# Kernel tuning notes

Hardware: AMD Instinct MI355X
Metric: run time of the kernel (lower is better)

The kernel has to match this reference:

```python
import jax, jax.numpy as jnp
import numpy as np

L, B, D = 2048, 8, 768
EPS_BN = 1e-5
EPS_LN = 1e-5
SCALE = 1.0 / float(np.sqrt(D))


def setup_inputs() -> dict:
    key = jax.random.key(0)
    ks = jax.random.split(key, 8)
    f32 = jnp.float32
    return {
        "x_a": jax.random.normal(ks[0], (L, B, D), dtype=f32),
        "x_v": jax.random.normal(ks[1], (L, B, D), dtype=f32),
        "x": jax.random.normal(ks[2], (L, B, D), dtype=f32),
        # conv1x1 (audio branch): weight [out_ch, in_ch], bias [out_ch]
        "W_a": jax.random.normal(ks[3], (D, D), dtype=f32) * 0.02,
        "b_a": jnp.zeros((D,), f32),
        "bn_a_g": jnp.ones((D,), f32),
        "bn_a_b": jnp.zeros((D,), f32),
        "prelu_a": jnp.full((1,), 0.25, f32),
        # conv1x1 (video branch)
        "W_v": jax.random.normal(ks[4], (D, D), dtype=f32) * 0.02,
        "b_v": jnp.zeros((D,), f32),
        "bn_v_g": jnp.ones((D,), f32),
        "bn_v_b": jnp.zeros((D,), f32),
        "prelu_v": jnp.full((1,), 0.25, f32),
        # final LayerNorm affine
        "ln_g": jnp.ones((D,), f32),
        "ln_b": jnp.zeros((D,), f32),
    }


def _branch(q, kv, W, b, bn_g, bn_b, alpha):
    # q: [B, L, D] queries; kv: [B, Lm, D] keys == values (cross-modal)
    attn = jax.nn.softmax(jnp.einsum('bld,bmd->blm', q, kv) * SCALE, axis=-1)
    ctx = jnp.einsum('blm,bmd->bld', attn, kv)            # [B, L, D]
    # Conv1d(kernel=1) over channel dim D == per-position linear
    y = jnp.einsum('bld,ed->ble', ctx, W) + b             # [B, L, D]
    # BatchNorm1d in training mode: batch stats over (B, L) per channel, biased var
    mean = jnp.mean(y, axis=(0, 1))
    var = jnp.var(y, axis=(0, 1))
    y = (y - mean) * jax.lax.rsqrt(var + EPS_BN) * bn_g + bn_b
    # PReLU (single shared alpha)
    return jnp.where(y > 0, y, alpha * y)


def reference(x_a, x_v, x, W_a, b_a, bn_a_g, bn_a_b, prelu_a,
              W_v, b_v, bn_v_g, bn_v_b, prelu_v, ln_g, ln_b):
    xa = jnp.swapaxes(x_a, 0, 1)   # [B, La, D]
    xv = jnp.swapaxes(x_v, 0, 1)   # [B, Lv, D]
    xq = jnp.swapaxes(x, 0, 1)     # [B, L, D]

    res_a = _branch(xq, xa, W_a, b_a, bn_a_g, bn_a_b, prelu_a)
    res_v = _branch(xq, xv, W_v, b_v, bn_v_g, bn_v_b, prelu_v)

    out = xq + res_a + res_v
    out = jnp.swapaxes(out, 0, 1)  # back to [L, B, D]

    mu = jnp.mean(out, axis=-1, keepdims=True)
    var = jnp.var(out, axis=-1, keepdims=True)
    return (out - mu) * jax.lax.rsqrt(var + EPS_LN) * ln_g + ln_b
```

## Files before the change

kernel.cpp:

```cpp
#include <hip/hip_runtime.h>
#include <stdint.h>

#define LL 2048
#define BB 8
#define DD 768
#define NROWS (LL*BB)
#define QKSCALE 0.03608439182435161f
#define EP 72

typedef __attribute__((ext_vector_type(8))) short short8;
typedef __attribute__((ext_vector_type(4))) float f32x4;
typedef unsigned short u16;
typedef unsigned int u32;

__device__ __forceinline__ float bf2f(u16 u) {
    union { u32 u; float f; } c; c.u = ((u32)u) << 16; return c.f;
}
__device__ __forceinline__ u16 f2bf(float f) {
    union { float f; u32 u; } c; c.f = f;
    return (u16)((c.u + 0x8000u) >> 16);
}

__global__ __launch_bounds__(256)
void cvt_kernel(const float* __restrict__ s0, u16* __restrict__ d0,
                const float* __restrict__ s1, u16* __restrict__ d1,
                const float* __restrict__ s2, u16* __restrict__ d2,
                const float* __restrict__ s3, u16* __restrict__ d3,
                const float* __restrict__ s4, u16* __restrict__ d4,
                int nbig4, int nsmall4)
{
    const float* src; u16* dst; int n4;
    switch (blockIdx.y) {
        case 0: src = s0; dst = d0; n4 = nbig4; break;
        case 1: src = s1; dst = d1; n4 = nbig4; break;
        case 2: src = s2; dst = d2; n4 = nbig4; break;
        case 3: src = s3; dst = d3; n4 = nsmall4; break;
        default: src = s4; dst = d4; n4 = nsmall4; break;
    }
    for (int i = blockIdx.x * 256 + threadIdx.x; i < n4; i += gridDim.x * 256) {
        float4 v = *(const float4*)&src[i * 4];
        ushort4 o;
        o.x = f2bf(v.x); o.y = f2bf(v.y); o.z = f2bf(v.z); o.w = f2bf(v.w);
        *(ushort4*)&dst[i * 4] = o;
    }
}

__device__ __forceinline__ void gll16(const u16* g, u16* l) {
    __builtin_amdgcn_global_load_lds((const __attribute__((address_space(1))) u32*)g,
                                     (__attribute__((address_space(3))) u32*)l, 16, 0, 0);
}

template<int EPI>
__global__ __launch_bounds__(512, 2)
void gemm_bt256(const u16* __restrict__ A, int lda, long astr,
                const u16* __restrict__ B, int ldb, long bstr,
                u16* __restrict__ C, long cstr, int ldc,
                int K, int sw,
                float* __restrict__ lsum,
                const float* __restrict__ bias,
                float* __restrict__ stats)
{
    __shared__ u16 lds[65536];

    const int tid = threadIdx.x;
    const int z = blockIdx.z;
    const int flat = blockIdx.y * gridDim.x + blockIdx.x;
    const int per = sw * gridDim.x;
    const int bm = (flat / per) * sw + (flat % sw);
    const int bn = (flat % per) / sw;
    const int m0 = bm * 256, n0 = bn * 256;

    const u16* Ab = A + (size_t)z * astr + (size_t)m0 * lda;
    const u16* Bb = B + (size_t)z * bstr + (size_t)n0 * ldb;
    u16* Cb = C + (size_t)z * cstr;

    const int lane = tid & 63, w = tid >> 6;
    const int wm = w >> 2, wn = w & 3;
    const int lr = lane & 15, lg = lane >> 4;

    const int ar0 = tid >> 2;
    const int ar1 = ar0 + 128;
    const int ag0 = (tid & 3) ^ ((ar0 >> 1) & 3);
    const int ag1 = (tid & 3) ^ ((ar1 >> 1) & 3);
    const u16* gA0 = Ab + (size_t)ar0 * lda + ag0 * 8;
    const u16* gA1 = Ab + (size_t)ar1 * lda + ag1 * 8;
    const u16* gB0 = Bb + (size_t)ar0 * ldb + ag0 * 8;
    const u16* gB1 = Bb + (size_t)ar1 * ldb + ag1 * 8;
    const int lA0 = tid * 8;
    const int lA1 = tid * 8 + 4096;
    const int lB0 = 8192 + tid * 8;
    const int lB1 = 12288 + tid * 8;

    const int swz = (lr >> 1) & 3;
    const int aoff = (wm * 128 + lr) * 32 + ((lg ^ swz) * 8);
    const int boff = 8192 + (wn * 64 + lr) * 32 + ((lg ^ swz) * 8);

    f32x4 acc[8][4];
    const f32x4 zz = {0.f, 0.f, 0.f, 0.f};
    #pragma unroll
    for (int i = 0; i < 8; ++i)
        #pragma unroll
        for (int j = 0; j < 4; ++j) acc[i][j] = zz;

    const int nt = K >> 5;

    {
        u16* b0 = lds;
        u16* b1 = lds + 16384;
        gll16(gA0, b0 + lA0); gll16(gA1, b0 + lA1);
        gll16(gB0, b0 + lB0); gll16(gB1, b0 + lB1);
        gll16(gA0 + 32, b1 + lA0); gll16(gA1 + 32, b1 + lA1);
        gll16(gB0 + 32, b1 + lB0); gll16(gB1 + 32, b1 + lB1);
    }
    asm volatile("s_waitcnt vmcnt(4)" ::: "memory");
    asm volatile("s_barrier" ::: "memory");

    for (int t = 0; t < nt; ++t) {
        const int cb = (t & 3) * 16384;
        const int sb = ((t + 2) & 3) * 16384;
        const int kt2 = (t + 2) * 32;
        const bool pre = (t + 2 < nt);
        short8 af[4], bf[4];

        #pragma unroll
        for (int mi = 0; mi < 4; ++mi) af[mi] = *(const short8*)&lds[cb + aoff + mi * 512];
        #pragma unroll
        for (int ni = 0; ni < 4; ++ni) bf[ni] = *(const short8*)&lds[cb + boff + ni * 512];
        if (pre) { gll16(gA0 + kt2, lds + sb + lA0); gll16(gA1 + kt2, lds + sb + lA1); }
        asm volatile("s_barrier" ::: "memory");
        __builtin_amdgcn_s_setprio(1);
        #pragma unroll
        for (int mi = 0; mi < 4; ++mi)
            #pragma unroll
            for (int ni = 0; ni < 4; ++ni)
                acc[mi][ni] = __builtin_amdgcn_mfma_f32_16x16x32_bf16(af[mi], bf[ni], acc[mi][ni], 0, 0, 0);
        __builtin_amdgcn_s_setprio(0);

        #pragma unroll
        for (int mi = 0; mi < 4; ++mi) af[mi] = *(const short8*)&lds[cb + aoff + 2048 + mi * 512];
        if (pre) { gll16(gB0 + kt2, lds + sb + lB0); gll16(gB1 + kt2, lds + sb + lB1); }
        if (t < nt - 2) asm volatile("s_waitcnt vmcnt(4)" ::: "memory");
        else            asm volatile("s_waitcnt vmcnt(0)" ::: "memory");
        asm volatile("s_barrier" ::: "memory");
        __builtin_amdgcn_s_setprio(1);
        #pragma unroll
        for (int mi = 0; mi < 4; ++mi)
            #pragma unroll
            for (int ni = 0; ni < 4; ++ni)
                acc[mi + 4][ni] = __builtin_amdgcn_mfma_f32_16x16x32_bf16(af[mi], bf[ni], acc[mi + 4][ni], 0, 0, 0);
        __builtin_amdgcn_s_setprio(0);
    }

    asm volatile("s_barrier" ::: "memory");
    u16* eb = lds + w * 4608;

    float invl[8][4]; float bcol[4];
    if constexpr (EPI == 2) {
        #pragma unroll
        for (int mi = 0; mi < 8; ++mi)
            #pragma unroll
            for (int r = 0; r < 4; ++r)
                invl[mi][r] = 1.0f / lsum[z * 2048 + m0 + wm * 128 + mi * 16 + lg * 4 + r];
        #pragma unroll
        for (int ni = 0; ni < 4; ++ni)
            bcol[ni] = bias[n0 + wn * 64 + ni * 16 + lr];
    }
    float csum[4] = {0, 0, 0, 0}, csq[4] = {0, 0, 0, 0};

    #pragma unroll
    for (int half = 0; half < 2; ++half) {
        #pragma unroll
        for (int mi = 0; mi < 4; ++mi) {
            const int MI = half * 4 + mi;
            float rsum[4] = {0, 0, 0, 0};
            #pragma unroll
            for (int ni = 0; ni < 4; ++ni) {
                #pragma unroll
                for (int r = 0; r < 4; ++r) {
                    float v = acc[MI][ni][r];
                    if constexpr (EPI == 1) { v = __expf(v * QKSCALE); rsum[r] += v; }
                    if constexpr (EPI == 2) { v = v * invl[MI][r] + bcol[ni]; csum[ni] += v; csq[ni] += v * v; }
                    eb[(mi * 16 + lg * 4 + r) * EP + ni * 16 + lr] = f2bf(v);
                }
            }
            if constexpr (EPI == 1) {
                #pragma unroll
                for (int r = 0; r < 4; ++r) {
                    float s = rsum[r];
                    s += __shfl_xor(s, 1); s += __shfl_xor(s, 2);
                    s += __shfl_xor(s, 4); s += __shfl_xor(s, 8);
                    if (lr == 0)
                        atomicAdd(&lsum[z * 2048 + m0 + wm * 128 + MI * 16 + lg * 4 + r], s);
                }
            }
        }
        #pragma unroll
        for (int c = 0; c < 8; ++c) {
            int row = c * 8 + (lane >> 3);
            short8 v = *(const short8*)&eb[row * EP + (lane & 7) * 8];
            *(short8*)&Cb[(size_t)(m0 + wm * 128 + half * 64 + row) * ldc + n0 + wn * 64 + (lane & 7) * 8] = v;
        }
    }
    if constexpr (EPI == 2) {
        #pragma unroll
        for (int ni = 0; ni < 4; ++ni) {
            float s = csum[ni], q = csq[ni];
            s += __shfl_xor(s, 16); s += __shfl_xor(s, 32);
            q += __shfl_xor(q, 16); q += __shfl_xor(q, 32);
            if (lg == 0) {
                atomicAdd(&stats[n0 + wn * 64 + ni * 16 + lr], s);
                atomicAdd(&stats[DD + n0 + wn * 64 + ni * 16 + lr], q);
            }
        }
    }
}

__global__ void bn_params(const float* __restrict__ stats_a, const float* __restrict__ stats_v,
                          const float* __restrict__ g_a, const float* __restrict__ be_a,
                          const float* __restrict__ g_v, const float* __restrict__ be_v,
                          float* __restrict__ bnp_a, float* __restrict__ bnp_v)
{
    const int e = threadIdx.x;
    const float* st = (blockIdx.x == 0) ? stats_a : stats_v;
    const float* g  = (blockIdx.x == 0) ? g_a  : g_v;
    const float* be = (blockIdx.x == 0) ? be_a : be_v;
    float* bnp = (blockIdx.x == 0) ? bnp_a : bnp_v;
    float mean = st[e] * (1.0f / NROWS);
    float var  = st[DD + e] * (1.0f / NROWS) - mean * mean;
    float scale = g[e] * rsqrtf(var + 1e-5f);
    bnp[e]      = scale;
    bnp[DD + e] = be[e] - mean * scale;
}

__global__ __launch_bounds__(256)
void final_kernel(const float* __restrict__ x,
                  const u16* __restrict__ y_a, const u16* __restrict__ y_v,
                  const float* __restrict__ bnp_a, const float* __restrict__ bnp_v,
                  const float* __restrict__ pra, const float* __restrict__ prv,
                  const float* __restrict__ lng, const float* __restrict__ lnb,
                  float* __restrict__ out)
{
    const int n = blockIdx.x;
    const int tid = threadIdx.x;
    __shared__ float vrow[DD];
    __shared__ float reds[4], reds2[4];
    const float aa = pra[0];
    const float av = prv[0];
    const size_t base = (size_t)n * DD;
    float s = 0.f, s2 = 0.f;
    for (int e = tid; e < DD; e += 256) {
        float ya = bf2f(y_a[base + e]) * bnp_a[e] + bnp_a[DD + e];
        ya = ya > 0.f ? ya : aa * ya;
        float yv = bf2f(y_v[base + e]) * bnp_v[e] + bnp_v[DD + e];
        yv = yv > 0.f ? yv : av * yv;
        float v = x[base + e] + ya + yv;
        vrow[e] = v;
        s += v; s2 += v * v;
    }
    for (int off = 32; off > 0; off >>= 1) { s += __shfl_xor(s, off); s2 += __shfl_xor(s2, off); }
    const int wv = tid >> 6;
    if ((tid & 63) == 0) { reds[wv] = s; reds2[wv] = s2; }
    __syncthreads();
    float ts  = reds[0] + reds[1] + reds[2] + reds[3];
    float ts2 = reds2[0] + reds2[1] + reds2[2] + reds2[3];
    float mean = ts * (1.0f / DD);
    float var  = ts2 * (1.0f / DD) - mean * mean;
    float rstd = rsqrtf(var + 1e-5f);
    for (int e = tid; e < DD; e += 256) {
        float o = (vrow[e] - mean) * rstd * lng[e] + lnb[e];
        out[base + e] = o;
    }
}

extern "C" void kernel_launch(void* const* d_in, const int* in_sizes, int n_in,
                              void* d_out, int out_size, void* d_ws, size_t ws_size,
                              hipStream_t stream)
{
    const float* x_a    = (const float*)d_in[0];
    const float* x_v    = (const float*)d_in[1];
    const float* x      = (const float*)d_in[2];
    const float* W_a    = (const float*)d_in[3];
    const float* b_a    = (const float*)d_in[4];
    const float* bn_a_g = (const float*)d_in[5];
    const float* bn_a_b = (const float*)d_in[6];
    const float* pr_a   = (const float*)d_in[7];
    const float* W_v    = (const float*)d_in[8];
    const float* b_v    = (const float*)d_in[9];
    const float* bn_v_g = (const float*)d_in[10];
    const float* bn_v_b = (const float*)d_in[11];
    const float* pr_v   = (const float*)d_in[12];
    const float* ln_g   = (const float*)d_in[13];
    const float* ln_b   = (const float*)d_in[14];

    float* stats_a = (float*)d_ws;
    float* stats_v = stats_a + 1536;
    float* bnp_a   = stats_v + 1536;
    float* bnp_v   = bnp_a + 1536;
    float* lsum    = bnp_v + 1536;
    u16* xq_bf = (u16*)(lsum + 16 * 2048);
    u16* xa_bf = xq_bf + (size_t)NROWS * DD;
    u16* xv_bf = xa_bf + (size_t)NROWS * DD;
    u16* Wa_bf = xv_bf + (size_t)NROWS * DD;
    u16* Wv_bf = Wa_bf + (size_t)DD * DD;
    u16* UT    = Wv_bf + (size_t)DD * DD;
    u16* y_a = xa_bf;
    u16* y_v = xv_bf;
    size_t fixed_bytes = (size_t)((char*)UT - (char*)d_ws);

    int nb = 1;
    for (int cand = 8; cand >= 1; cand >>= 1) {
        size_t need = fixed_bytes + (size_t)cand * (3145728ull + 8388608ull);
        if (need <= ws_size) { nb = cand; break; }
    }
    u16* P = UT + (size_t)nb * (768 * 2048);

    hipMemsetAsync(stats_a, 0, (4 * 1536 + 16 * 2048) * sizeof(float), stream);

    cvt_kernel<<<dim3(3072, 5), 256, 0, stream>>>(
        x, xq_bf, x_a, xa_bf, x_v, xv_bf, W_a, Wa_bf, W_v, Wv_bf,
        NROWS * DD / 4, DD * DD / 4);

    const u16*   KVs[2]   = { xa_bf, xv_bf };
    const u16*   Ws[2]    = { Wa_bf, Wv_bf };
    const float* BIs[2]   = { b_a, b_v };
    u16*         Ys[2]    = { y_a, y_v };
    float*       STs[2]   = { stats_a, stats_v };

    for (int br = 0; br < 2; ++br) {
        const u16* kv = KVs[br];
        for (int c0 = 0; c0 < 8; c0 += nb) {
            float* lsum_bc = (nb == 8) ? (lsum + br * 8 * 2048) : lsum;
            if (nb != 8)
                hipMemsetAsync(lsum, 0, (size_t)nb * 2048 * sizeof(float), stream);
            gemm_bt256<0><<<dim3(8, 3, nb), 512, 0, stream>>>(
                Ws[br], DD, 0, kv + c0 * DD, BB * DD, DD,
                UT, (long)768 * 2048, 2048, DD, 3, nullptr, nullptr, nullptr);
            gemm_bt256<1><<<dim3(8, 8, nb), 512, 0, stream>>>(
                xq_bf + c0 * DD, BB * DD, DD, kv + c0 * DD, BB * DD, DD,
                P, (long)2048 * 2048, 2048, DD, 4, lsum_bc, nullptr, nullptr);
            gemm_bt256<2><<<dim3(3, 8, nb), 512, 0, stream>>>(
                P, 2048, (long)2048 * 2048, UT, 2048, (long)768 * 2048,
                Ys[br] + (size_t)c0 * DD, DD, BB * DD, 2048, 4, lsum_bc, BIs[br], STs[br]);
        }
    }

    bn_params<<<2, 768, 0, stream>>>(stats_a, stats_v, bn_a_g, bn_a_b, bn_v_g, bn_v_b, bnp_a, bnp_v);
    final_kernel<<<NROWS, 256, 0, stream>>>(x, y_a, y_v, bnp_a, bnp_v, pr_a, pr_v, ln_g, ln_b,
                                            (float*)d_out);
}
```

Measured before the change: 539.3 us.

## Software-pipeline LDS fragment loads across k-steps and drop one barrier

```diff
diff --git a/kernel.cpp b/kernel.cpp
--- a/kernel.cpp
+++ b/kernel.cpp
@@ -104,6 +104,8 @@
 
     const int nt = K >> 5;
 
+    short8 a1[4], a2[4], bE[4], bO[4];
+
     {
         u16* b0 = lds;
         u16* b1 = lds + 16384;
@@ -114,42 +116,60 @@
     }
     asm volatile("s_waitcnt vmcnt(4)" ::: "memory");
     asm volatile("s_barrier" ::: "memory");
-
-    for (int t = 0; t < nt; ++t) {
-        const int cb = (t & 3) * 16384;
-        const int sb = ((t + 2) & 3) * 16384;
-        const int kt2 = (t + 2) * 32;
-        const bool pre = (t + 2 < nt);
-        short8 af[4], bf[4];
-
-        #pragma unroll
-        for (int mi = 0; mi < 4; ++mi) af[mi] = *(const short8*)&lds[cb + aoff + mi * 512];
-        #pragma unroll
-        for (int ni = 0; ni < 4; ++ni) bf[ni] = *(const short8*)&lds[cb + boff + ni * 512];
-        if (pre) { gll16(gA0 + kt2, lds + sb + lA0); gll16(gA1 + kt2, lds + sb + lA1); }
-        asm volatile("s_barrier" ::: "memory");
-        __builtin_amdgcn_s_setprio(1);
-        #pragma unroll
-        for (int mi = 0; mi < 4; ++mi)
-            #pragma unroll
-            for (int ni = 0; ni < 4; ++ni)
-                acc[mi][ni] = __builtin_amdgcn_mfma_f32_16x16x32_bf16(af[mi], bf[ni], acc[mi][ni], 0, 0, 0);
-        __builtin_amdgcn_s_setprio(0);
-
-        #pragma unroll
-        for (int mi = 0; mi < 4; ++mi) af[mi] = *(const short8*)&lds[cb + aoff + 2048 + mi * 512];
-        if (pre) { gll16(gB0 + kt2, lds + sb + lB0); gll16(gB1 + kt2, lds + sb + lB1); }
-        if (t < nt - 2) asm volatile("s_waitcnt vmcnt(4)" ::: "memory");
-        else            asm volatile("s_waitcnt vmcnt(0)" ::: "memory");
-        asm volatile("s_barrier" ::: "memory");
-        __builtin_amdgcn_s_setprio(1);
-        #pragma unroll
-        for (int mi = 0; mi < 4; ++mi)
-            #pragma unroll
-            for (int ni = 0; ni < 4; ++ni)
-                acc[mi + 4][ni] = __builtin_amdgcn_mfma_f32_16x16x32_bf16(af[mi], bf[ni], acc[mi + 4][ni], 0, 0, 0);
-        __builtin_amdgcn_s_setprio(0);
-    }
+    #pragma unroll
+    for (int mi = 0; mi < 4; ++mi) a1[mi] = *(const short8*)&lds[aoff + mi * 512];
+    #pragma unroll
+    for (int ni = 0; ni < 4; ++ni) bE[ni] = *(const short8*)&lds[boff + ni * 512];
+
+#define TILE_STEP(T, BC, BN)                                                            \
+    {                                                                                   \
+        const int cb_ = ((T) & 3) * 16384;                                              \
+        const int sb_ = (((T) + 2) & 3) * 16384;                                        \
+        const int kt2_ = ((T) + 2) * 32;                                                \
+        _Pragma("unroll")                                                               \
+        for (int mi = 0; mi < 4; ++mi)                                                  \
+            a2[mi] = *(const short8*)&lds[cb_ + aoff + 2048 + mi * 512];                \
+        if ((T) + 2 < nt) {                                                             \
+            gll16(gA0 + kt2_, lds + sb_ + lA0);                                         \
+            gll16(gA1 + kt2_, lds + sb_ + lA1);                                         \
+        }                                                                               \
+        __builtin_amdgcn_s_setprio(1);                                                  \
+        _Pragma("unroll")                                                               \
+        for (int mi = 0; mi < 4; ++mi)                                                  \
+            _Pragma("unroll")                                                           \
+            for (int ni = 0; ni < 4; ++ni)                                              \
+                acc[mi][ni] = __builtin_amdgcn_mfma_f32_16x16x32_bf16(a1[mi], BC[ni], acc[mi][ni], 0, 0, 0); \
+        __builtin_amdgcn_s_setprio(0);                                                  \
+        if ((T) + 2 < nt) {                                                             \
+            gll16(gB0 + kt2_, lds + sb_ + lB0);                                         \
+            gll16(gB1 + kt2_, lds + sb_ + lB1);                                         \
+        }                                                                               \
+        if ((T) < nt - 2) { asm volatile("s_waitcnt vmcnt(4)" ::: "memory"); }          \
+        else              { asm volatile("s_waitcnt vmcnt(0)" ::: "memory"); }          \
+        asm volatile("s_barrier" ::: "memory");                                         \
+        if ((T) + 1 < nt) {                                                             \
+            const int nb_ = (((T) + 1) & 3) * 16384;                                    \
+            _Pragma("unroll")                                                           \
+            for (int mi = 0; mi < 4; ++mi)                                              \
+                a1[mi] = *(const short8*)&lds[nb_ + aoff + mi * 512];                   \
+            _Pragma("unroll")                                                           \
+            for (int ni = 0; ni < 4; ++ni)                                              \
+                BN[ni] = *(const short8*)&lds[nb_ + boff + ni * 512];                   \
+        }                                                                               \
+        __builtin_amdgcn_s_setprio(1);                                                  \
+        _Pragma("unroll")                                                               \
+        for (int mi = 0; mi < 4; ++mi)                                                  \
+            _Pragma("unroll")                                                           \
+            for (int ni = 0; ni < 4; ++ni)                                              \
+                acc[mi + 4][ni] = __builtin_amdgcn_mfma_f32_16x16x32_bf16(a2[mi], BC[ni], acc[mi + 4][ni], 0, 0, 0); \
+        __builtin_amdgcn_s_setprio(0);                                                  \
+    }
+
+    for (int t = 0; t < nt; t += 2) {
+        TILE_STEP(t, bE, bO)
+        TILE_STEP(t + 1, bO, bE)
+    }
+#undef TILE_STEP
 
     asm volatile("s_barrier" ::: "memory");
     u16* eb = lds + w * 4608;
```

Measured after the change: 571.0 us. 5.9% more time.

## Shrink GEMM tile to 256x128 with 4 waves and double-buffered LDS

Applied to the files above, without the earlier changes.

```diff
diff --git a/kernel.cpp b/kernel.cpp
--- a/kernel.cpp
+++ b/kernel.cpp
@@ -51,7 +51,7 @@
 }
 
 template<int EPI>
-__global__ __launch_bounds__(512, 2)
+__global__ __launch_bounds__(256, 3)
 void gemm_bt256(const u16* __restrict__ A, int lda, long astr,
                 const u16* __restrict__ B, int ldb, long bstr,
                 u16* __restrict__ C, long cstr, int ldc,
@@ -60,7 +60,7 @@
                 const float* __restrict__ bias,
                 float* __restrict__ stats)
 {
-    __shared__ u16 lds[65536];
+    __shared__ u16 lds[24576];
 
     const int tid = threadIdx.x;
     const int z = blockIdx.z;
@@ -68,32 +68,26 @@
     const int per = sw * gridDim.x;
     const int bm = (flat / per) * sw + (flat % sw);
     const int bn = (flat % per) / sw;
-    const int m0 = bm * 256, n0 = bn * 256;
+    const int m0 = bm * 256, n0 = bn * 128;
 
     const u16* Ab = A + (size_t)z * astr + (size_t)m0 * lda;
     const u16* Bb = B + (size_t)z * bstr + (size_t)n0 * ldb;
     u16* Cb = C + (size_t)z * cstr;
 
     const int lane = tid & 63, w = tid >> 6;
-    const int wm = w >> 2, wn = w & 3;
+    const int wm = w >> 1, wn = w & 1;
     const int lr = lane & 15, lg = lane >> 4;
 
-    const int ar0 = tid >> 2;
-    const int ar1 = ar0 + 128;
-    const int ag0 = (tid & 3) ^ ((ar0 >> 1) & 3);
-    const int ag1 = (tid & 3) ^ ((ar1 >> 1) & 3);
-    const u16* gA0 = Ab + (size_t)ar0 * lda + ag0 * 8;
-    const u16* gA1 = Ab + (size_t)ar1 * lda + ag1 * 8;
-    const u16* gB0 = Bb + (size_t)ar0 * ldb + ag0 * 8;
-    const u16* gB1 = Bb + (size_t)ar1 * ldb + ag1 * 8;
-    const int lA0 = tid * 8;
-    const int lA1 = tid * 8 + 4096;
-    const int lB0 = 8192 + tid * 8;
-    const int lB1 = 12288 + tid * 8;
-
-    const int swz = (lr >> 1) & 3;
-    const int aoff = (wm * 128 + lr) * 32 + ((lg ^ swz) * 8);
-    const int boff = 8192 + (wn * 64 + lr) * 32 + ((lg ^ swz) * 8);
+    const int arow = tid >> 2;
+    const int gsw = (tid & 3) ^ (arow & 3);
+    const u16* pA = Ab + (size_t)arow * lda + gsw * 8;
+    const u16* pB = Bb + (size_t)arow * ldb + gsw * 8;
+    const size_t lda64 = (size_t)64 * lda;
+    const size_t ldb64 = (size_t)64 * ldb;
+
+    const int slot = lg ^ (lr & 3);
+    const int aof = (wm * 128 + lr) * 32 + slot * 8;
+    const int bof = 8192 + (wn * 64 + lr) * 32 + slot * 8;
 
     f32x4 acc[8][4];
     const f32x4 zz = {0.f, 0.f, 0.f, 0.f};
@@ -104,54 +98,38 @@
 
     const int nt = K >> 5;
 
-    {
-        u16* b0 = lds;
-        u16* b1 = lds + 16384;
-        gll16(gA0, b0 + lA0); gll16(gA1, b0 + lA1);
-        gll16(gB0, b0 + lB0); gll16(gB1, b0 + lB1);
-        gll16(gA0 + 32, b1 + lA0); gll16(gA1 + 32, b1 + lA1);
-        gll16(gB0 + 32, b1 + lB0); gll16(gB1 + 32, b1 + lB1);
-    }
-    asm volatile("s_waitcnt vmcnt(4)" ::: "memory");
+#define STAGE(KT, BUF)                                                   \
+    do {                                                                 \
+        gll16(pA + (KT),              lds + (BUF) + tid * 8);            \
+        gll16(pA + (KT) + lda64,      lds + (BUF) + 2048 + tid * 8);     \
+        gll16(pA + (KT) + 2 * lda64,  lds + (BUF) + 4096 + tid * 8);     \
+        gll16(pA + (KT) + 3 * lda64,  lds + (BUF) + 6144 + tid * 8);     \
+        gll16(pB + (KT),              lds + (BUF) + 8192 + tid * 8);     \
+        gll16(pB + (KT) + ldb64,      lds + (BUF) + 10240 + tid * 8);    \
+    } while (0)
+
+    STAGE(0, 0);
+    asm volatile("s_waitcnt vmcnt(0)" ::: "memory");
     asm volatile("s_barrier" ::: "memory");
 
     for (int t = 0; t < nt; ++t) {
-        const int cb = (t & 3) * 16384;
-        const int sb = ((t + 2) & 3) * 16384;
-        const int kt2 = (t + 2) * 32;
-        const bool pre = (t + 2 < nt);
-        short8 af[4], bf[4];
-
-        #pragma unroll
-        for (int mi = 0; mi < 4; ++mi) af[mi] = *(const short8*)&lds[cb + aoff + mi * 512];
-        #pragma unroll
-        for (int ni = 0; ni < 4; ++ni) bf[ni] = *(const short8*)&lds[cb + boff + ni * 512];
-        if (pre) { gll16(gA0 + kt2, lds + sb + lA0); gll16(gA1 + kt2, lds + sb + lA1); }
-        asm volatile("s_barrier" ::: "memory");
-        __builtin_amdgcn_s_setprio(1);
-        #pragma unroll
-        for (int mi = 0; mi < 4; ++mi)
+        const int cb = (t & 1) * 12288;
+        if (t + 1 < nt) STAGE((t + 1) * 32, 12288 - cb);
+        short8 af[8], bf[4];
+        #pragma unroll
+        for (int mi = 0; mi < 8; ++mi) af[mi] = *(const short8*)&lds[cb + aof + mi * 512];
+        #pragma unroll
+        for (int ni = 0; ni < 4; ++ni) bf[ni] = *(const short8*)&lds[cb + bof + ni * 512];
+        #pragma unroll
+        for (int mi = 0; mi < 8; ++mi)
             #pragma unroll
             for (int ni = 0; ni < 4; ++ni)
                 acc[mi][ni] = __builtin_amdgcn_mfma_f32_16x16x32_bf16(af[mi], bf[ni], acc[mi][ni], 0, 0, 0);
-        __builtin_amdgcn_s_setprio(0);
-
-        #pragma unroll
-        for (int mi = 0; mi < 4; ++mi) af[mi] = *(const short8*)&lds[cb + aoff + 2048 + mi * 512];
-        if (pre) { gll16(gB0 + kt2, lds + sb + lB0); gll16(gB1 + kt2, lds + sb + lB1); }
-        if (t < nt - 2) asm volatile("s_waitcnt vmcnt(4)" ::: "memory");
-        else            asm volatile("s_waitcnt vmcnt(0)" ::: "memory");
+        asm volatile("s_waitcnt vmcnt(0)" ::: "memory");
         asm volatile("s_barrier" ::: "memory");
-        __builtin_amdgcn_s_setprio(1);
-        #pragma unroll
-        for (int mi = 0; mi < 4; ++mi)
-            #pragma unroll
-            for (int ni = 0; ni < 4; ++ni)
-                acc[mi + 4][ni] = __builtin_amdgcn_mfma_f32_16x16x32_bf16(af[mi], bf[ni], acc[mi + 4][ni], 0, 0, 0);
-        __builtin_amdgcn_s_setprio(0);
-    }
-
-    asm volatile("s_barrier" ::: "memory");
+    }
+#undef STAGE
+
     u16* eb = lds + w * 4608;
 
     float invl[8][4]; float bcol[4];
@@ -332,13 +310,13 @@
             float* lsum_bc = (nb == 8) ? (lsum + br * 8 * 2048) : lsum;
             if (nb != 8)
                 hipMemsetAsync(lsum, 0, (size_t)nb * 2048 * sizeof(float), stream);
-            gemm_bt256<0><<<dim3(8, 3, nb), 512, 0, stream>>>(
+            gemm_bt256<0><<<dim3(16, 3, nb), 256, 0, stream>>>(
                 Ws[br], DD, 0, kv + c0 * DD, BB * DD, DD,
                 UT, (long)768 * 2048, 2048, DD, 3, nullptr, nullptr, nullptr);
-            gemm_bt256<1><<<dim3(8, 8, nb), 512, 0, stream>>>(
+            gemm_bt256<1><<<dim3(16, 8, nb), 256, 0, stream>>>(
                 xq_bf + c0 * DD, BB * DD, DD, kv + c0 * DD, BB * DD, DD,
                 P, (long)2048 * 2048, 2048, DD, 4, lsum_bc, nullptr, nullptr);
-            gemm_bt256<2><<<dim3(3, 8, nb), 512, 0, stream>>>(
+            gemm_bt256<2><<<dim3(6, 8, nb), 256, 0, stream>>>(
                 P, 2048, (long)2048 * 2048, UT, 2048, (long)768 * 2048,
                 Ys[br] + (size_t)c0 * DD, DD, BB * DD, 2048, 4, lsum_bc, BIs[br], STs[br]);
         }
```

New measurement: 581.6 us. +7.9%, slower.
